# Optimization experiments

Measured on AMD Instinct MI355X. Metric: run time of the kernel, lower is better.

The kernel has to match this reference:

```python
import jax, jax.numpy as jnp
import numpy as np

B, L, I, H, C, E = 32, 2048, 512, 512, 512, 512
TEMP = 0.5
EPS = 1e-20


def setup_inputs() -> dict:
    key = jax.random.key(0)
    ks = jax.random.split(key, 8)
    s_in = 1.0 / np.sqrt(I)
    s_h = 1.0 / np.sqrt(H)
    s_c = 1.0 / np.sqrt(C)
    return {
        "inputs_BxLxI": jax.random.normal(ks[0], (B, L, I), dtype=jnp.float32),
        "W_h": jax.random.uniform(ks[1], (H, I), jnp.float32, -s_in, s_in),
        "b_h": jax.random.uniform(ks[2], (H,), jnp.float32, -s_in, s_in),
        "W_logits": jax.random.uniform(ks[3], (C, H), jnp.float32, -s_h, s_h),
        "b_logits": jax.random.uniform(ks[4], (C,), jnp.float32, -s_h, s_h),
        "codebook_CxE": jax.random.uniform(ks[5], (C, E), jnp.float32, -s_c, s_c),
        "u_noise": jax.random.uniform(ks[6], (B, L, C), dtype=jnp.float32),
        "testing": 0,
    }


def reference(inputs_BxLxI, W_h, b_h, W_logits, b_logits, codebook_CxE, u_noise, testing):
    # 1-layer MLP before quantization
    hiddens = jax.nn.relu(jnp.einsum('bli,hi->blh', inputs_BxLxI, W_h) + b_h)
    logits_BxLxC = jnp.einsum('blh,ch->blc', hiddens, W_logits) + b_logits

    if testing:
        ind = jnp.argmax(logits_BxLxC, axis=-1)
        onehot_BxLxC = jax.nn.one_hot(ind, C, dtype=logits_BxLxC.dtype)
    else:
        # gumbel-softmax with straight-through one-hot
        g = -jnp.log(-jnp.log(u_noise + EPS) + EPS)
        y = jax.nn.softmax((logits_BxLxC + g) / TEMP, axis=-1)
        ind = jnp.argmax(y, axis=-1)
        y_hard = jax.nn.one_hot(ind, C, dtype=y.dtype)
        onehot_BxLxC = jax.lax.stop_gradient(y_hard - y) + y

    # disguised embedding gather: onehot @ codebook
    codes_BxLxE = jnp.einsum('blc,ce->ble', onehot_BxLxC, codebook_CxE)
    return (logits_BxLxC, codes_BxLxE)
```

## Files before the change

kernel.cpp:

```cpp
#include <hip/hip_runtime.h>
#include <hip/hip_fp16.h>

typedef _Float16 h16;
typedef __attribute__((ext_vector_type(8))) _Float16 h16x8;
typedef __attribute__((ext_vector_type(4))) _Float16 h16x4;
typedef __attribute__((ext_vector_type(4))) float f32x4;

#define KDIM 512
#define NDIM 512
#define LO_SCALE 4096.0f
#define LO_INV   0.000244140625f

__device__ __forceinline__ void gload16(const void* g, void* l) {
  __builtin_amdgcn_global_load_lds((const __attribute__((address_space(1))) void*)g,
                                   (__attribute__((address_space(3))) void*)l, 16, 0, 0);
}

#define WAITV(n) asm volatile("s_waitcnt vmcnt(" #n ")" ::: "memory")
#define WAITL0() asm volatile("s_waitcnt lgkmcnt(0)" ::: "memory")
#define SB() __builtin_amdgcn_sched_barrier(0)

__global__ void split_w(const float* __restrict__ Wh, const float* __restrict__ Wl,
                        h16* __restrict__ WhHi, h16* __restrict__ WhLo,
                        h16* __restrict__ WlHi, h16* __restrict__ WlLo) {
  int i = blockIdx.x * 256 + threadIdx.x;
  float a = Wh[i];
  h16 h = (h16)a;
  WhHi[i] = h; WhLo[i] = (h16)((a - (float)h) * LO_SCALE);
  a = Wl[i];
  h = (h16)a;
  WlHi[i] = h; WlLo[i] = (h16)((a - (float)h) * LO_SCALE);
}

__launch_bounds__(512, 2)
__global__ void gemm6_k(const float* __restrict__ X,
                        const h16* __restrict__ BHi, const h16* __restrict__ BLo,
                        const float* __restrict__ bias,
                        h16* __restrict__ OHi, h16* __restrict__ OLo) {
  __shared__ __align__(16) char lds[147456];
  const int tid = threadIdx.x;
  const int wave = tid >> 6, lane = tid & 63;
  const int wn = wave;
  const long arow0 = (long)blockIdx.x * 64;
  const int q = lane >> 4, rlo = lane & 15;

  f32x4 acc_hh[4][4] = {};
  f32x4 acc_mx[4][4] = {};
  f32x4 areg[2];

  const int axrow = tid >> 3;
  const int ajb = (tid & 7) * 8;
  const int asw = ((axrow & 1) << 6) | (((axrow >> 1) & 3) << 4);

  auto aload = [&](f32x4& ar, int kt) {
    ar = *(const f32x4*)((const char*)X + (arow0 + axrow) * 2048 +
                         (long)kt * 128 + (tid & 7) * 16);
  };
  auto awrite = [&](const f32x4& ar, char* buf) {
    h16x4 hv, lv;
#pragma unroll
    for (int e = 0; e < 4; ++e) {
      h16 h = (h16)ar[e];
      hv[e] = h;
      lv[e] = (h16)((ar[e] - (float)h) * LO_SCALE);
    }
    *(h16x4*)(buf + axrow * 128 + (ajb ^ asw)) = hv;
    *(h16x4*)(buf + axrow * 128 + ((ajb + 64) ^ asw)) = lv;
  };
  auto bgld = [&](char* buf, int kt) {
#pragma unroll
    for (int pass = 0; pass < 8; ++pass) {
      int p = pass * 8192 + wave * 1024 + lane * 16;
      int row = p >> 7;
      int gs = ((p >> 4) & 7) ^ (row & 7);
      const char* sp = (gs & 4) ? (const char*)BLo : (const char*)BHi;
      long off = (long)row * 1024 + (long)kt * 64 + (gs & 3) * 16;
      gload16(sp + off, buf + 8192 + pass * 8192 + wave * 1024);
    }
  };

  aload(areg[0], 0);
  aload(areg[1], 1);
  WAITV(1);
  awrite(areg[0], lds);
  bgld(lds, 0);
  WAITV(8);
  awrite(areg[1], lds + 73728);
  aload(areg[0], 2);
  bgld(lds + 73728, 1);
  WAITL0();

#pragma unroll
  for (int t = 0; t < 16; ++t) {
    if (t <= 13) { WAITV(9); } else if (t == 14) { WAITV(8); } else { WAITV(0); }
    SB();
    __builtin_amdgcn_s_barrier();
    SB();

    if (t <= 12) aload(areg[(t + 3) & 1], t + 3);

    char* buf = lds + (t & 1) * 73728;
    h16x8 ah[4], al[4], bh[4], bl[4];
#pragma unroll
    for (int i = 0; i < 4; ++i) {
      int row = i * 16 + rlo;
      int swa = ((row & 1) << 6) | (((row >> 1) & 3) << 4);
      ah[i] = *(const h16x8*)(buf + row * 128 + ((q * 16) ^ swa));
      al[i] = *(const h16x8*)(buf + row * 128 + ((q * 16 + 64) ^ swa));
      int rb = wn * 64 + i * 16 + rlo;
      int swb = (rb & 7) << 4;
      bh[i] = *(const h16x8*)(buf + 8192 + rb * 128 + ((q * 16) ^ swb));
      bl[i] = *(const h16x8*)(buf + 8192 + rb * 128 + ((q * 16 + 64) ^ swb));
    }
#pragma unroll
    for (int i = 0; i < 4; ++i)
#pragma unroll
      for (int j = 0; j < 4; ++j)
        acc_hh[i][j] = __builtin_amdgcn_mfma_f32_16x16x32_f16(ah[i], bh[j], acc_hh[i][j], 0, 0, 0);
#pragma unroll
    for (int i = 0; i < 4; ++i)
#pragma unroll
      for (int j = 0; j < 4; ++j)
        acc_mx[i][j] = __builtin_amdgcn_mfma_f32_16x16x32_f16(ah[i], bl[j], acc_mx[i][j], 0, 0, 0);
#pragma unroll
    for (int i = 0; i < 4; ++i)
#pragma unroll
      for (int j = 0; j < 4; ++j)
        acc_mx[i][j] = __builtin_amdgcn_mfma_f32_16x16x32_f16(al[i], bh[j], acc_mx[i][j], 0, 0, 0);

    WAITL0();
    SB();
    __builtin_amdgcn_s_barrier();
    SB();
    if (t <= 12) {
      WAITV(9);
      awrite(areg[(t + 2) & 1], lds + (t & 1) * 73728);
      bgld(lds + (t & 1) * 73728, t + 2);
    } else if (t == 13) {
      WAITV(8);
      awrite(areg[1], lds + 73728);
      bgld(lds + 73728, 15);
    }
  }

#pragma unroll
  for (int j = 0; j < 4; ++j) {
    int lcol = wn * 64 + j * 16 + rlo;
    float bv = bias[lcol];
#pragma unroll
    for (int i = 0; i < 4; ++i)
#pragma unroll
      for (int r = 0; r < 4; ++r) {
        int lrow = i * 16 + q * 4 + r;
        float v = fmaxf(acc_hh[i][j][r] + acc_mx[i][j][r] * LO_INV + bv, 0.0f);
        h16 h = (h16)v;
        h16 l = (h16)((v - (float)h) * LO_SCALE);
        unsigned uu = (unsigned)__builtin_bit_cast(unsigned short, h) |
                      ((unsigned)__builtin_bit_cast(unsigned short, l) << 16);
        *(unsigned*)(lds + lrow * 2048 + lcol * 4) = uu;
      }
  }
  __syncthreads();
#pragma unroll
  for (int pass = 0; pass < 16; ++pass) {
    int o = pass * 8192 + tid * 16;
    int lrow = o >> 11;
    int lcb = o & 2047;
    uint4 d = *(const uint4*)(lds + o);
    uint2 hi, lo;
    hi.x = (d.x & 0xffffu) | (d.y << 16);
    hi.y = (d.z & 0xffffu) | (d.w << 16);
    lo.x = (d.x >> 16) | (d.y & 0xffff0000u);
    lo.y = (d.z >> 16) | (d.w & 0xffff0000u);
    long gb = (arow0 + lrow) * 1024 + (lcb >> 1);
    *(uint2*)((char*)OHi + gb) = hi;
    *(uint2*)((char*)OLo + gb) = lo;
  }
}

template <int EPI>
__launch_bounds__(256, 2)
__global__ void gemm4_k(const h16* __restrict__ AHi, const h16* __restrict__ ALo,
                        const h16* __restrict__ BHi, const h16* __restrict__ BLo,
                        const float* __restrict__ bias,
                        float* __restrict__ Cf32,
                        h16* __restrict__ OHi, h16* __restrict__ OLo) {
  __shared__ __align__(16) char lds[65536];
  const int tid = threadIdx.x;
  const int wave = tid >> 6, lane = tid & 63;
  const int wg = (blockIdx.x & 7) * 256 + (blockIdx.x >> 3);
  const int bm = wg >> 2, bn = wg & 3;
  const int wm = wave >> 1, wn = wave & 1;
  const long arow0 = (long)bm * 128;
  const int brow0 = bn * 128;
  const int q = lane >> 4, rlo = lane & 15;

  f32x4 acc_hh[4][4] = {};
  f32x4 acc_mx[4][4] = {};

#define STAGE4(bufoff, kt)                                                    \
  {                                                                           \
    _Pragma("unroll")                                                         \
    for (int pass = 0; pass < 4; ++pass) {                                    \
      int p = pass * 4096 + wave * 1024 + lane * 16;                          \
      int row = p >> 7;                                                       \
      int gs = ((p >> 4) & 7) ^ (row & 7);                                    \
      const char* sp = (gs & 4) ? (const char*)ALo : (const char*)AHi;        \
      long off = (arow0 + row) * 1024 + (kt) * 64 + (gs & 3) * 16;            \
      gload16(sp + off, lds + (bufoff) + pass * 4096 + wave * 1024);          \
    }                                                                         \
    _Pragma("unroll")                                                         \
    for (int pass = 0; pass < 4; ++pass) {                                    \
      int p = pass * 4096 + wave * 1024 + lane * 16;                          \
      int row = p >> 7;                                                       \
      int gs = ((p >> 4) & 7) ^ (row & 7);                                    \
      const char* sp = (gs & 4) ? (const char*)BLo : (const char*)BHi;        \
      long off = (long)(brow0 + row) * 1024 + (kt) * 64 + (gs & 3) * 16;      \
      gload16(sp + off, lds + (bufoff) + 16384 + pass * 4096 + wave * 1024);  \
    }                                                                         \
  }

  STAGE4(0, 0);
  STAGE4(32768, 1);

#pragma unroll
  for (int t = 0; t < 16; ++t) {
    if (t < 15) { WAITV(8); } else { WAITV(0); }
    SB();
    __builtin_amdgcn_s_barrier();
    SB();

    const char* buf = lds + (t & 1) * 32768;
    h16x8 ah[4], al[4], bh[4], bl[4];
#pragma unroll
    for (int i = 0; i < 4; ++i) {
      int row = wm * 64 + i * 16 + rlo;
      int sw = (row & 7) << 4;
      ah[i] = *(const h16x8*)(buf + row * 128 + ((q * 16) ^ sw));
      al[i] = *(const h16x8*)(buf + row * 128 + ((q * 16 + 64) ^ sw));
      int rb = wn * 64 + i * 16 + rlo;
      int swb = (rb & 7) << 4;
      bh[i] = *(const h16x8*)(buf + 16384 + rb * 128 + ((q * 16) ^ swb));
      bl[i] = *(const h16x8*)(buf + 16384 + rb * 128 + ((q * 16 + 64) ^ swb));
    }
#pragma unroll
    for (int i = 0; i < 4; ++i)
#pragma unroll
      for (int j = 0; j < 4; ++j)
        acc_hh[i][j] = __builtin_amdgcn_mfma_f32_16x16x32_f16(ah[i], bh[j], acc_hh[i][j], 0, 0, 0);
#pragma unroll
    for (int i = 0; i < 4; ++i)
#pragma unroll
      for (int j = 0; j < 4; ++j)
        acc_mx[i][j] = __builtin_amdgcn_mfma_f32_16x16x32_f16(ah[i], bl[j], acc_mx[i][j], 0, 0, 0);
#pragma unroll
    for (int i = 0; i < 4; ++i)
#pragma unroll
      for (int j = 0; j < 4; ++j)
        acc_mx[i][j] = __builtin_amdgcn_mfma_f32_16x16x32_f16(al[i], bh[j], acc_mx[i][j], 0, 0, 0);

    WAITL0();
    SB();
    __builtin_amdgcn_s_barrier();
    SB();
    if (t + 2 < 16) STAGE4((t & 1) * 32768, t + 2);
  }
#undef STAGE4

#pragma unroll
  for (int j = 0; j < 4; ++j) {
    int lcol = wn * 64 + j * 16 + rlo;
    float bv = bias[bn * 128 + lcol];
#pragma unroll
    for (int i = 0; i < 4; ++i)
#pragma unroll
      for (int r = 0; r < 4; ++r) {
        int lrow = wm * 64 + i * 16 + q * 4 + r;
        float v = acc_hh[i][j][r] + acc_mx[i][j][r] * LO_INV + bv;
        if (EPI == 0) {
          v = fmaxf(v, 0.0f);
          h16 h = (h16)v;
          h16 l = (h16)((v - (float)h) * LO_SCALE);
          unsigned uu = (unsigned)__builtin_bit_cast(unsigned short, h) |
                        ((unsigned)__builtin_bit_cast(unsigned short, l) << 16);
          *(unsigned*)(lds + lrow * 512 + lcol * 4) = uu;
        } else {
          *(float*)(lds + lrow * 512 + lcol * 4) = v;
        }
      }
  }
  __syncthreads();
#pragma unroll
  for (int pass = 0; pass < 16; ++pass) {
    int o = pass * 4096 + tid * 16;
    int lrow = o >> 9;
    int lcb = o & 511;
    if (EPI == 0) {
      uint4 d = *(const uint4*)(lds + o);
      uint2 hi, lo;
      hi.x = (d.x & 0xffffu) | (d.y << 16);
      hi.y = (d.z & 0xffffu) | (d.w << 16);
      lo.x = (d.x >> 16) | (d.y & 0xffff0000u);
      lo.y = (d.z >> 16) | (d.w & 0xffff0000u);
      long gb = (arow0 + lrow) * 1024 + bn * 256 + (lcb >> 1);
      *(uint2*)((char*)OHi + gb) = hi;
      *(uint2*)((char*)OLo + gb) = lo;
    } else {
      f32x4 d = *(const f32x4*)(lds + o);
      long gb = (arow0 + lrow) * 2048 + bn * 512 + lcb;
      *(f32x4*)((char*)Cf32 + gb) = d;
    }
  }
}

__global__ void k3_argmax_gather(const float* __restrict__ logits,
                                 const float* __restrict__ u,
                                 const float* __restrict__ cb,
                                 const int* __restrict__ testing,
                                 float* __restrict__ codes) {
  const int wave = threadIdx.x >> 6, lane = threadIdx.x & 63;
  const long row = (long)blockIdx.x * 4 + wave;
  const f32x4* lrow = (const f32x4*)(logits + row * 512);
  const f32x4* urow = (const f32x4*)(u + row * 512);
  const int test = *testing;

  float best = -3.4e38f;
  int bi = 0;
#pragma unroll
  for (int h = 0; h < 2; ++h) {
    int c4 = h * 64 + lane;
    f32x4 z = lrow[c4];
    if (!test) {
      f32x4 uu = urow[c4];
#pragma unroll
      for (int t = 0; t < 4; ++t)
        z[t] += -logf(-logf(uu[t] + 1e-20f) + 1e-20f);
    }
#pragma unroll
    for (int t = 0; t < 4; ++t) {
      int c = c4 * 4 + t;
      if (z[t] > best) { best = z[t]; bi = c; }
    }
  }
#pragma unroll
  for (int off = 32; off; off >>= 1) {
    float ob = __shfl_xor(best, off);
    int oi = __shfl_xor(bi, off);
    if (ob > best || (ob == best && oi < bi)) { best = ob; bi = oi; }
  }
  const f32x4* src = (const f32x4*)(cb + (long)bi * 512);
  f32x4* dst = (f32x4*)(codes + row * 512);
  dst[lane] = src[lane];
  dst[lane + 64] = src[lane + 64];
}

extern "C" void kernel_launch(void* const* d_in, const int* in_sizes, int n_in,
                              void* d_out, int out_size, void* d_ws, size_t ws_size,
                              hipStream_t stream) {
  const float* X = (const float*)d_in[0];
  const float* Wh = (const float*)d_in[1];
  const float* bh = (const float*)d_in[2];
  const float* Wl = (const float*)d_in[3];
  const float* bl = (const float*)d_in[4];
  const float* cb = (const float*)d_in[5];
  const float* u = (const float*)d_in[6];
  const int* testing = (const int*)d_in[7];

  float* logits = (float*)d_out;
  float* codes = logits + 33554432;
  h16* Hhi = (h16*)codes;
  h16* Hlo = Hhi + 33554432;

  h16* WhHi = (h16*)d_ws;
  h16* WhLo = WhHi + 262144;
  h16* WlHi = WhLo + 262144;
  h16* WlLo = WlHi + 262144;

  split_w<<<dim3(1024), dim3(256), 0, stream>>>(Wh, Wl, WhHi, WhLo, WlHi, WlLo);

  gemm6_k<<<dim3(1024), dim3(512), 0, stream>>>(X, WhHi, WhLo, bh, Hhi, Hlo);

  gemm4_k<1><<<dim3(2048), dim3(256), 0, stream>>>(Hhi, Hlo, WlHi, WlLo, bl,
                                                   logits, nullptr, nullptr);

  k3_argmax_gather<<<dim3(16384), dim3(256), 0, stream>>>(logits, u, cb, testing, codes);
}
```

Measured before the change: 318.2 us.

## Split first GEMM N dimension across two blocks with 256-thread workgroups

The first GEMM kernel now uses 256-thread blocks that each compute a 64x256 output tile instead of 512-thread blocks computing 64x512, doubling the grid to 2048 with an XCD-aware block remap. LDS use per block drops from 144 KB to 80 KB. The intent is better occupancy and scheduling on the CUs. The cost is that each X tile is loaded and split into fp16 hi/lo parts twice, once per N half.

```diff
diff --git a/kernel.cpp b/kernel.cpp
--- a/kernel.cpp
+++ b/kernel.cpp
@@ -32,74 +32,82 @@
   WlHi[i] = h; WlLo[i] = (h16)((a - (float)h) * LO_SCALE);
 }
 
-__launch_bounds__(512, 2)
-__global__ void gemm6_k(const float* __restrict__ X,
+__launch_bounds__(256, 2)
+__global__ void gemm7_k(const float* __restrict__ X,
                         const h16* __restrict__ BHi, const h16* __restrict__ BLo,
                         const float* __restrict__ bias,
                         h16* __restrict__ OHi, h16* __restrict__ OLo) {
-  __shared__ __align__(16) char lds[147456];
+  __shared__ __align__(16) char lds[81920];
   const int tid = threadIdx.x;
   const int wave = tid >> 6, lane = tid & 63;
   const int wn = wave;
-  const long arow0 = (long)blockIdx.x * 64;
+  const int wg = (blockIdx.x & 7) * 256 + (blockIdx.x >> 3);
+  const int bm = wg >> 1, bn = wg & 1;
+  const long arow0 = (long)bm * 64;
+  const int brow0 = bn * 256;
   const int q = lane >> 4, rlo = lane & 15;
 
   f32x4 acc_hh[4][4] = {};
   f32x4 acc_mx[4][4] = {};
-  f32x4 areg[2];
-
-  const int axrow = tid >> 3;
-  const int ajb = (tid & 7) * 8;
+  f32x4 areg[2][2];
+
+  const int axrow = tid >> 2;
+  const int akb = (tid & 3) * 32;
+  const int ajb = (tid & 3) * 16;
   const int asw = ((axrow & 1) << 6) | (((axrow >> 1) & 3) << 4);
 
-  auto aload = [&](f32x4& ar, int kt) {
-    ar = *(const f32x4*)((const char*)X + (arow0 + axrow) * 2048 +
-                         (long)kt * 128 + (tid & 7) * 16);
+  auto aload = [&](f32x4 (&ar)[2], int kt) {
+    const char* base = (const char*)X + (arow0 + axrow) * 2048 + (long)kt * 128 + akb;
+    ar[0] = *(const f32x4*)base;
+    ar[1] = *(const f32x4*)(base + 16);
   };
-  auto awrite = [&](const f32x4& ar, char* buf) {
-    h16x4 hv, lv;
-#pragma unroll
-    for (int e = 0; e < 4; ++e) {
-      h16 h = (h16)ar[e];
-      hv[e] = h;
-      lv[e] = (h16)((ar[e] - (float)h) * LO_SCALE);
-    }
-    *(h16x4*)(buf + axrow * 128 + (ajb ^ asw)) = hv;
-    *(h16x4*)(buf + axrow * 128 + ((ajb + 64) ^ asw)) = lv;
+  auto awrite = [&](const f32x4 (&ar)[2], char* buf) {
+    h16x8 hv, lv;
+#pragma unroll
+    for (int p = 0; p < 2; ++p)
+#pragma unroll
+      for (int e = 0; e < 4; ++e) {
+        float a = ar[p][e];
+        h16 h = (h16)a;
+        hv[p * 4 + e] = h;
+        lv[p * 4 + e] = (h16)((a - (float)h) * LO_SCALE);
+      }
+    *(h16x8*)(buf + axrow * 128 + (ajb ^ asw)) = hv;
+    *(h16x8*)(buf + axrow * 128 + ((ajb + 64) ^ asw)) = lv;
   };
   auto bgld = [&](char* buf, int kt) {
 #pragma unroll
     for (int pass = 0; pass < 8; ++pass) {
-      int p = pass * 8192 + wave * 1024 + lane * 16;
+      int p = pass * 4096 + tid * 16;
       int row = p >> 7;
       int gs = ((p >> 4) & 7) ^ (row & 7);
       const char* sp = (gs & 4) ? (const char*)BLo : (const char*)BHi;
-      long off = (long)row * 1024 + (long)kt * 64 + (gs & 3) * 16;
-      gload16(sp + off, buf + 8192 + pass * 8192 + wave * 1024);
+      long off = (long)(brow0 + row) * 1024 + (long)kt * 64 + (gs & 3) * 16;
+      gload16(sp + off, buf + 8192 + pass * 4096 + wave * 1024);
     }
   };
 
   aload(areg[0], 0);
   aload(areg[1], 1);
-  WAITV(1);
+  WAITV(2);
   awrite(areg[0], lds);
   bgld(lds, 0);
   WAITV(8);
-  awrite(areg[1], lds + 73728);
+  awrite(areg[1], lds + 40960);
   aload(areg[0], 2);
-  bgld(lds + 73728, 1);
+  bgld(lds + 40960, 1);
   WAITL0();
 
 #pragma unroll
   for (int t = 0; t < 16; ++t) {
-    if (t <= 13) { WAITV(9); } else if (t == 14) { WAITV(8); } else { WAITV(0); }
+    if (t <= 13) { WAITV(10); } else if (t == 14) { WAITV(8); } else { WAITV(0); }
     SB();
     __builtin_amdgcn_s_barrier();
     SB();
 
     if (t <= 12) aload(areg[(t + 3) & 1], t + 3);
 
-    char* buf = lds + (t & 1) * 73728;
+    char* buf = lds + (t & 1) * 40960;
     h16x8 ah[4], al[4], bh[4], bl[4];
 #pragma unroll
     for (int i = 0; i < 4; ++i) {
@@ -133,20 +141,20 @@
     __builtin_amdgcn_s_barrier();
     SB();
     if (t <= 12) {
-      WAITV(9);
-      awrite(areg[(t + 2) & 1], lds + (t & 1) * 73728);
-      bgld(lds + (t & 1) * 73728, t + 2);
+      WAITV(10);
+      awrite(areg[(t + 2) & 1], lds + (t & 1) * 40960);
+      bgld(lds + (t & 1) * 40960, t + 2);
     } else if (t == 13) {
       WAITV(8);
-      awrite(areg[1], lds + 73728);
-      bgld(lds + 73728, 15);
+      awrite(areg[1], lds + 40960);
+      bgld(lds + 40960, 15);
     }
   }
 
 #pragma unroll
   for (int j = 0; j < 4; ++j) {
     int lcol = wn * 64 + j * 16 + rlo;
-    float bv = bias[lcol];
+    float bv = bias[bn * 256 + lcol];
 #pragma unroll
     for (int i = 0; i < 4; ++i)
 #pragma unroll
@@ -157,22 +165,22 @@
         h16 l = (h16)((v - (float)h) * LO_SCALE);
         unsigned uu = (unsigned)__builtin_bit_cast(unsigned short, h) |
                       ((unsigned)__builtin_bit_cast(unsigned short, l) << 16);
-        *(unsigned*)(lds + lrow * 2048 + lcol * 4) = uu;
+        *(unsigned*)(lds + lrow * 1024 + lcol * 4) = uu;
       }
   }
   __syncthreads();
 #pragma unroll
   for (int pass = 0; pass < 16; ++pass) {
-    int o = pass * 8192 + tid * 16;
-    int lrow = o >> 11;
-    int lcb = o & 2047;
+    int o = pass * 4096 + tid * 16;
+    int lrow = o >> 10;
+    int lcb = o & 1023;
     uint4 d = *(const uint4*)(lds + o);
     uint2 hi, lo;
     hi.x = (d.x & 0xffffu) | (d.y << 16);
     hi.y = (d.z & 0xffffu) | (d.w << 16);
     lo.x = (d.x >> 16) | (d.y & 0xffff0000u);
     lo.y = (d.z >> 16) | (d.w & 0xffff0000u);
-    long gb = (arow0 + lrow) * 1024 + (lcb >> 1);
+    long gb = (arow0 + lrow) * 1024 + bn * 512 + (lcb >> 1);
     *(uint2*)((char*)OHi + gb) = hi;
     *(uint2*)((char*)OLo + gb) = lo;
   }
@@ -378,7 +386,7 @@
 
   split_w<<<dim3(1024), dim3(256), 0, stream>>>(Wh, Wl, WhHi, WhLo, WlHi, WlLo);
 
-  gemm6_k<<<dim3(1024), dim3(512), 0, stream>>>(X, WhHi, WhLo, bh, Hhi, Hlo);
+  gemm7_k<<<dim3(2048), dim3(256), 0, stream>>>(X, WhHi, WhLo, bh, Hhi, Hlo);
 
   gemm4_k<1><<<dim3(2048), dim3(256), 0, stream>>>(Hhi, Hlo, WlHi, WlLo, bl,
                                                    logits, nullptr, nullptr);
```

New measurement: 311.6 us. 2.1% less time.
